# Kernel optimization log

Hardware: AMD Instinct MI355X
Metric: run time of the kernel (lower is better)

Reference implementation:

```python
import jax, jax.numpy as jnp
import numpy as np
from jax.scipy.special import logsumexp
from jax import lax

TARGET_SIZE = 50
TAG_SIZE = TARGET_SIZE + 2  # +2 for START/END tags


def setup_inputs() -> dict:
    key = jax.random.key(0)
    k1, k2 = jax.random.split(key)
    B, L, T = 1024, 512, TAG_SIZE
    feats = jax.random.normal(k1, (B, L, T), dtype=jnp.float32)
    mask = jnp.ones((B, L), dtype=jnp.int32)
    # transitions init per CRF.__init__: zeros, with transitions[:, START]=-1000
    # and transitions[END, :]=-1000 (START=T-2, END=T-1). Add small noise to the
    # trainable part so gradients are non-trivial.
    trans = 0.1 * jax.random.normal(k2, (T, T), dtype=jnp.float32)
    trans = trans.at[:, T - 2].set(-1000.0)  # nothing transitions INTO start
    trans = trans.at[T - 1, :].set(-1000.0)  # nothing transitions OUT of end
    return {"feats": feats, "mask": mask, "transitions": trans}


def reference(feats, mask, transitions):
    # feats: (B, L, T), mask: (B, L) int, transitions: (T, T)
    B, L, T = feats.shape
    START, END = T - 2, T - 1
    # scores[t, b, i, j] = feats[b, t, j] + transitions[i, j]
    # initial partition = scores[0, :, START, :]
    partition0 = feats[:, 0, :] + transitions[START, :]  # (B, T)

    feats_t = jnp.swapaxes(feats[:, 1:, :], 0, 1)   # (L-1, B, T)
    mask_t = jnp.swapaxes(mask[:, 1:], 0, 1)        # (L-1, B)

    def step(part, xs):
        f_t, m_t = xs  # (B, T), (B,)
        # cur[b, i, j] = feats[b,t,j] + transitions[i,j] + partition[b,i]
        cur = f_t[:, None, :] + transitions[None, :, :] + part[:, :, None]
        cur_part = logsumexp(cur, axis=1)  # reduce over previous tag i -> (B, T)
        part = jnp.where((m_t > 0)[:, None], cur_part, part)
        return part, None

    partition, _ = lax.scan(step, partition0, (feats_t, mask_t))

    # final transition step, then select END tag
    final_vals = transitions[None, :, :] + partition[:, :, None]  # (B, T, T)
    final_partition = logsumexp(final_vals, axis=1)[:, END]       # (B,)
    return final_partition.sum()
```

## Files before the change

### kernel.cpp

```cpp
#include <hip/hip_runtime.h>


#define TT 52
#define LL 512
#define NS 8

__device__ __forceinline__ float rl(float x, int lane) {
    return __int_as_float(__builtin_amdgcn_readlane(__float_as_int(x), lane));
}

__global__ void __launch_bounds__(64)
__attribute__((amdgpu_waves_per_eu(1, 1)))
crf_fwd(
    const float* __restrict__ feats,
    const int*   __restrict__ mask,
    const float* __restrict__ trans,
    float*       __restrict__ out)
{
    __shared__ __align__(16) float plds[64];

    const int b = blockIdx.x;
    const int j = threadIdx.x;
    const bool act = (j < TT);
    const int jc = act ? j : 0;

    const float* fb = feats + (size_t)b * LL * TT;
    const int*   mb = mask  + (size_t)b * LL;

    float E[TT];
#pragma unroll
    for (int i = 0; i < TT; ++i) {
        float e = __expf(trans[i * TT + jc]);
        E[i] = act ? e : 0.0f;
    }

    float part0 = act ? (fb[j] + trans[(TT - 2) * TT + j]) : -1.0e30f;
    float shift = rl(part0, 0);
    float pv = act ? __expf(part0 - shift) : 0.0f;

    plds[j] = pv;

    const float4* pq = (const float4*)plds;

    float fpre[NS];
    int   mc[NS];
#pragma unroll
    for (int u = 0; u < NS; ++u) {
        int t = 1 + u;
        fpre[u] = fb[t * TT + jc];
        mc[u]   = mb[t];
    }

    for (int t0 = 1; t0 + NS <= LL; t0 += NS) {
        float fnx[NS];
        int   mn[NS];
#pragma unroll
        for (int u = 0; u < NS; ++u) {
            int tn = t0 + NS + u;
            int tcl = tn < LL ? tn : (LL - 1);
            fnx[u] = fb[tcl * TT + jc];
            mn[u]  = mb[tcl];
        }

        float ef[NS];
#pragma unroll
        for (int u = 0; u < NS; ++u) ef[u] = __expf(fpre[u]);

#pragma unroll
        for (int u = 0; u < NS; ++u) {
            float a0 = 0.f, a1 = 0.f, a2 = 0.f, a3 = 0.f;
#pragma unroll
            for (int k = 0; k < TT / 4; ++k) {
                float4 q = pq[k];
                a0 = fmaf(q.x, E[4 * k + 0], a0);
                a1 = fmaf(q.y, E[4 * k + 1], a1);
                a2 = fmaf(q.z, E[4 * k + 2], a2);
                a3 = fmaf(q.w, E[4 * k + 3], a3);
            }
            float pn = ((a0 + a1) + (a2 + a3)) * ef[u];
            pv = (mc[u] > 0) ? pn : pv;
            if (u == NS - 1) {
                float c = rl(pv, 0);
                shift += __logf(c);
                pv *= __builtin_amdgcn_rcpf(c);
            }
            plds[j] = pv;
        }
#pragma unroll
        for (int u = 0; u < NS; ++u) { fpre[u] = fnx[u]; mc[u] = mn[u]; }
    }

#pragma unroll
    for (int u = 0; u < 7; ++u) {
        float efu = __expf(fpre[u]);
        float a0 = 0.f, a1 = 0.f, a2 = 0.f, a3 = 0.f;
#pragma unroll
        for (int k = 0; k < TT / 4; ++k) {
            float4 q = pq[k];
            a0 = fmaf(q.x, E[4 * k + 0], a0);
            a1 = fmaf(q.y, E[4 * k + 1], a1);
            a2 = fmaf(q.z, E[4 * k + 2], a2);
            a3 = fmaf(q.w, E[4 * k + 3], a3);
        }
        float pn = ((a0 + a1) + (a2 + a3)) * efu;
        pv = (mc[u] > 0) ? pn : pv;
        plds[j] = pv;
    }

    float eend = __expf(trans[jc * TT + (TT - 1)]);
    float val = act ? (eend * pv) : 0.0f;
#pragma unroll
    for (int o = 32; o >= 1; o >>= 1)
        val += __shfl_xor(val, o, 64);
    if (j == 0) atomicAdd(out, __logf(val) + shift);
}

extern "C" void kernel_launch(void* const* d_in, const int* in_sizes, int n_in,
                              void* d_out, int out_size, void* d_ws, size_t ws_size,
                              hipStream_t stream) {
    const float* feats = (const float*)d_in[0];
    const int*   mask  = (const int*)d_in[1];
    const float* trans = (const float*)d_in[2];
    float* out = (float*)d_out;

    const int B = in_sizes[1] / LL;

    hipMemsetAsync(d_out, 0, sizeof(float), stream);
    crf_fwd<<<B, 64, 0, stream>>>(feats, mask, trans, out);
}
```

Baseline: 248.0 us.

## Split CRF recurrence into concurrent forward and backward half-chains meeting at midpoint

Runs the forward partition recurrence and a backward (beta) recurrence at the same time, each covering about half of the sequence, and combines them with a dot product at the midpoint. This halves the serial dependency chain length and gives two independent FMA streams per step to hide LDS and ALU latency. In exchange it doubles the register-held transition matrix (column and row copies), increasing VGPR pressure. It also assumes the backward mask handling matches the reference semantics, which holds for an all-ones mask.

```diff
diff --git a/kernel.cpp b/kernel.cpp
--- a/kernel.cpp
+++ b/kernel.cpp
@@ -17,7 +17,7 @@
     const float* __restrict__ trans,
     float*       __restrict__ out)
 {
-    __shared__ __align__(16) float plds[64];
+    __shared__ __align__(16) float plds[128];
 
     const int b = blockIdx.x;
     const int j = threadIdx.x;
@@ -27,92 +27,150 @@
     const float* fb = feats + (size_t)b * LL * TT;
     const int*   mb = mask  + (size_t)b * LL;
 
-    float E[TT];
+    float Ecol[TT], Erow[TT];
 #pragma unroll
     for (int i = 0; i < TT; ++i) {
-        float e = __expf(trans[i * TT + jc]);
-        E[i] = act ? e : 0.0f;
+        float ec = __expf(trans[i * TT + jc]);
+        float er = __expf(trans[jc * TT + i]);
+        Ecol[i] = act ? ec : 0.0f;
+        Erow[i] = act ? er : 0.0f;
     }
 
     float part0 = act ? (fb[j] + trans[(TT - 2) * TT + j]) : -1.0e30f;
-    float shift = rl(part0, 0);
-    float pv = act ? __expf(part0 - shift) : 0.0f;
+    float shiftF = rl(part0, 0);
+    float pvF = act ? __expf(part0 - shiftF) : 0.0f;
 
-    plds[j] = pv;
+    float wv = act ? __expf(trans[jc * TT + (TT - 1)]) : 0.0f;
+    float shiftB = 0.0f;
 
-    const float4* pq = (const float4*)plds;
+    const float4* pqF = (const float4*)plds;
+    const float4* pqB = (const float4*)(plds + 64);
 
-    float fpre[NS];
-    int   mc[NS];
+    float fpF[NS], fpB[NS];
+    int   mcF[NS], mcB[NS];
 #pragma unroll
     for (int u = 0; u < NS; ++u) {
-        int t = 1 + u;
-        fpre[u] = fb[t * TT + jc];
-        mc[u]   = mb[t];
+        fpF[u] = fb[(1 + u) * TT + jc];
+        mcF[u] = mb[1 + u];
+        fpB[u] = fb[(LL - 1 - u) * TT + jc];
+        mcB[u] = mb[LL - 1 - u];
     }
 
-    for (int t0 = 1; t0 + NS <= LL; t0 += NS) {
-        float fnx[NS];
-        int   mn[NS];
+    for (int g = 0; g + NS <= 248; g += NS) {
+        float fnF[NS], fnB[NS];
+        int   mnF[NS], mnB[NS];
 #pragma unroll
         for (int u = 0; u < NS; ++u) {
-            int tn = t0 + NS + u;
-            int tcl = tn < LL ? tn : (LL - 1);
-            fnx[u] = fb[tcl * TT + jc];
-            mn[u]  = mb[tcl];
+            int kn = g + NS + u;
+            fnF[u] = fb[(1 + kn) * TT + jc];
+            mnF[u] = mb[1 + kn];
+            fnB[u] = fb[(LL - 1 - kn) * TT + jc];
+            mnB[u] = mb[LL - 1 - kn];
         }
 
-        float ef[NS];
+        float efF[NS], efB[NS];
 #pragma unroll
-        for (int u = 0; u < NS; ++u) ef[u] = __expf(fpre[u]);
+        for (int u = 0; u < NS; ++u) {
+            efF[u] = __expf(fpF[u]);
+            efB[u] = __expf(fpB[u]);
+        }
 
 #pragma unroll
         for (int u = 0; u < NS; ++u) {
+            plds[j]      = pvF;
+            plds[64 + j] = efB[u] * wv;
             float a0 = 0.f, a1 = 0.f, a2 = 0.f, a3 = 0.f;
+            float b0 = 0.f, b1 = 0.f, b2 = 0.f, b3 = 0.f;
 #pragma unroll
-            for (int k = 0; k < TT / 4; ++k) {
-                float4 q = pq[k];
-                a0 = fmaf(q.x, E[4 * k + 0], a0);
-                a1 = fmaf(q.y, E[4 * k + 1], a1);
-                a2 = fmaf(q.z, E[4 * k + 2], a2);
-                a3 = fmaf(q.w, E[4 * k + 3], a3);
+            for (int kq = 0; kq < TT / 4; ++kq) {
+                float4 qf = pqF[kq];
+                float4 qb = pqB[kq];
+                a0 = fmaf(qf.x, Ecol[4 * kq + 0], a0);
+                a1 = fmaf(qf.y, Ecol[4 * kq + 1], a1);
+                a2 = fmaf(qf.z, Ecol[4 * kq + 2], a2);
+                a3 = fmaf(qf.w, Ecol[4 * kq + 3], a3);
+                b0 = fmaf(qb.x, Erow[4 * kq + 0], b0);
+                b1 = fmaf(qb.y, Erow[4 * kq + 1], b1);
+                b2 = fmaf(qb.z, Erow[4 * kq + 2], b2);
+                b3 = fmaf(qb.w, Erow[4 * kq + 3], b3);
             }
-            float pn = ((a0 + a1) + (a2 + a3)) * ef[u];
-            pv = (mc[u] > 0) ? pn : pv;
+            float pnF = ((a0 + a1) + (a2 + a3)) * efF[u];
+            float wnB = ((b0 + b1) + (b2 + b3));
+            pvF = (mcF[u] > 0) ? pnF : pvF;
+            wv  = (mcB[u] > 0) ? wnB : wv;
             if (u == NS - 1) {
-                float c = rl(pv, 0);
-                shift += __logf(c);
-                pv *= __builtin_amdgcn_rcpf(c);
+                float cF = rl(pvF, 0);
+                float cB = rl(wv, 0);
+                shiftF += __logf(cF);
+                shiftB += __logf(cB);
+                pvF *= __builtin_amdgcn_rcpf(cF);
+                wv  *= __builtin_amdgcn_rcpf(cB);
             }
-            plds[j] = pv;
         }
 #pragma unroll
-        for (int u = 0; u < NS; ++u) { fpre[u] = fnx[u]; mc[u] = mn[u]; }
+        for (int u = 0; u < NS; ++u) {
+            fpF[u] = fnF[u]; mcF[u] = mnF[u];
+            fpB[u] = fnB[u]; mcB[u] = mnB[u];
+        }
     }
 
 #pragma unroll
     for (int u = 0; u < 7; ++u) {
-        float efu = __expf(fpre[u]);
+        float efFu = __expf(fpF[u]);
+        float efBu = __expf(fpB[u]);
+        plds[j]      = pvF;
+        plds[64 + j] = efBu * wv;
+        float a0 = 0.f, a1 = 0.f, a2 = 0.f, a3 = 0.f;
+        float b0 = 0.f, b1 = 0.f, b2 = 0.f, b3 = 0.f;
+#pragma unroll
+        for (int kq = 0; kq < TT / 4; ++kq) {
+            float4 qf = pqF[kq];
+            float4 qb = pqB[kq];
+            a0 = fmaf(qf.x, Ecol[4 * kq + 0], a0);
+            a1 = fmaf(qf.y, Ecol[4 * kq + 1], a1);
+            a2 = fmaf(qf.z, Ecol[4 * kq + 2], a2);
+            a3 = fmaf(qf.w, Ecol[4 * kq + 3], a3);
+            b0 = fmaf(qb.x, Erow[4 * kq + 0], b0);
+            b1 = fmaf(qb.y, Erow[4 * kq + 1], b1);
+            b2 = fmaf(qb.z, Erow[4 * kq + 2], b2);
+            b3 = fmaf(qb.w, Erow[4 * kq + 3], b3);
+        }
+        float pnF = ((a0 + a1) + (a2 + a3)) * efFu;
+        float wnB = ((b0 + b1) + (b2 + b3));
+        pvF = (mcF[u] > 0) ? pnF : pvF;
+        wv  = (mcB[u] > 0) ? wnB : wv;
+    }
+
+    {
+        float cF = rl(pvF, 0);
+        float cB = rl(wv, 0);
+        shiftF += __logf(cF);
+        shiftB += __logf(cB);
+        pvF *= __builtin_amdgcn_rcpf(cF);
+        wv  *= __builtin_amdgcn_rcpf(cB);
+    }
+
+    {
+        float efFu = __expf(fpF[7]);
+        plds[j] = pvF;
         float a0 = 0.f, a1 = 0.f, a2 = 0.f, a3 = 0.f;
 #pragma unroll
-        for (int k = 0; k < TT / 4; ++k) {
-            float4 q = pq[k];
-            a0 = fmaf(q.x, E[4 * k + 0], a0);
-            a1 = fmaf(q.y, E[4 * k + 1], a1);
-            a2 = fmaf(q.z, E[4 * k + 2], a2);
-            a3 = fmaf(q.w, E[4 * k + 3], a3);
+        for (int kq = 0; kq < TT / 4; ++kq) {
+            float4 qf = pqF[kq];
+            a0 = fmaf(qf.x, Ecol[4 * kq + 0], a0);
+            a1 = fmaf(qf.y, Ecol[4 * kq + 1], a1);
+            a2 = fmaf(qf.z, Ecol[4 * kq + 2], a2);
+            a3 = fmaf(qf.w, Ecol[4 * kq + 3], a3);
         }
-        float pn = ((a0 + a1) + (a2 + a3)) * efu;
-        pv = (mc[u] > 0) ? pn : pv;
-        plds[j] = pv;
+        float pnF = ((a0 + a1) + (a2 + a3)) * efFu;
+        pvF = (mcF[7] > 0) ? pnF : pvF;
     }
 
-    float eend = __expf(trans[jc * TT + (TT - 1)]);
-    float val = act ? (eend * pv) : 0.0f;
+    float val = act ? (pvF * wv) : 0.0f;
 #pragma unroll
     for (int o = 32; o >= 1; o >>= 1)
         val += __shfl_xor(val, o, 64);
-    if (j == 0) atomicAdd(out, __logf(val) + shift);
+    if (j == 0) atomicAdd(out, __logf(val) + shiftF + shiftB);
 }
 
 extern "C" void kernel_launch(void* const* d_in, const int* in_sizes, int n_in,
```

Measured after the change: 243.5 us. Within noise of the previous version (-1.8%).

## Split CRF forward recursion into concurrent forward and backward halves per sequence

Applied to the files above, without the earlier changes.

Each block now runs two wavefronts: one runs the forward recursion over the first half of the sequence, and the other runs a backward (beta) recursion from the END tag over the second half using transposed transitions. The two partial vectors are combined with a dot product after a block barrier. This halves the serial dependency chain per sequence so that two independent chains share a SIMD. In exchange, the block needs twice the threads and registers, and masked-step handling in the backward half relies on the mask being a prefix.

```diff
diff --git a/kernel.cpp b/kernel.cpp
--- a/kernel.cpp
+++ b/kernel.cpp
@@ -4,115 +4,185 @@
 #define TT 52
 #define LL 512
 #define NS 8
+#define KSPLIT 256
 
 __device__ __forceinline__ float rl(float x, int lane) {
     return __int_as_float(__builtin_amdgcn_readlane(__float_as_int(x), lane));
 }
 
-__global__ void __launch_bounds__(64)
-__attribute__((amdgpu_waves_per_eu(1, 1)))
+__global__ void __launch_bounds__(128)
+__attribute__((amdgpu_waves_per_eu(2, 2)))
 crf_fwd(
     const float* __restrict__ feats,
     const int*   __restrict__ mask,
     const float* __restrict__ trans,
     float*       __restrict__ out)
 {
-    __shared__ __align__(16) float plds[64];
-
-    const int b = blockIdx.x;
-    const int j = threadIdx.x;
+    __shared__ __align__(16) float plds[2][64];
+    __shared__ float shsh[2];
+
+    const int b   = blockIdx.x;
+    const int tid = threadIdx.x;
+    const int w   = tid >> 6;
+    const int j   = tid & 63;
     const bool act = (j < TT);
     const int jc = act ? j : 0;
 
     const float* fb = feats + (size_t)b * LL * TT;
     const int*   mb = mask  + (size_t)b * LL;
 
-    float E[TT];
-#pragma unroll
-    for (int i = 0; i < TT; ++i) {
-        float e = __expf(trans[i * TT + jc]);
-        E[i] = act ? e : 0.0f;
+    float pv;
+    float shift;
+
+    if (w == 0) {
+        float E[TT];
+#pragma unroll
+        for (int i = 0; i < TT; ++i) {
+            float e = __expf(trans[i * TT + jc]);
+            E[i] = act ? e : 0.0f;
+        }
+
+        float part0 = act ? (fb[j] + trans[(TT - 2) * TT + j]) : -1.0e30f;
+        shift = rl(part0, 0);
+        pv = act ? __expf(part0 - shift) : 0.0f;
+        plds[0][j] = pv;
+
+        const float4* pq = (const float4*)plds[0];
+
+        float fpre[NS]; int mc[NS];
+#pragma unroll
+        for (int u = 0; u < NS; ++u) {
+            fpre[u] = fb[(1 + u) * TT + jc];
+            mc[u]   = mb[1 + u];
+        }
+
+        for (int t0 = 1; t0 + NS <= KSPLIT + 1; t0 += NS) {
+            float fnx[NS]; int mn[NS];
+#pragma unroll
+            for (int u = 0; u < NS; ++u) {
+                int tn = t0 + NS + u;
+                fnx[u] = fb[tn * TT + jc];
+                mn[u]  = mb[tn];
+            }
+            float ef[NS];
+#pragma unroll
+            for (int u = 0; u < NS; ++u) ef[u] = __expf(fpre[u]);
+
+#pragma unroll
+            for (int u = 0; u < NS; ++u) {
+                float a0 = 0.f, a1 = 0.f, a2 = 0.f, a3 = 0.f;
+#pragma unroll
+                for (int kq = 0; kq < TT / 4; ++kq) {
+                    float4 q = pq[kq];
+                    a0 = fmaf(q.x, E[4 * kq + 0], a0);
+                    a1 = fmaf(q.y, E[4 * kq + 1], a1);
+                    a2 = fmaf(q.z, E[4 * kq + 2], a2);
+                    a3 = fmaf(q.w, E[4 * kq + 3], a3);
+                }
+                float pn = ((a0 + a1) + (a2 + a3)) * ef[u];
+                pv = (mc[u] > 0) ? pn : pv;
+                if (u == NS - 1) {
+                    float c = rl(pv, 0);
+                    shift += __logf(c);
+                    pv *= __builtin_amdgcn_rcpf(c);
+                }
+                plds[0][j] = pv;
+            }
+#pragma unroll
+            for (int u = 0; u < NS; ++u) { fpre[u] = fnx[u]; mc[u] = mn[u]; }
+        }
+    } else {
+        float E[TT];
+#pragma unroll
+        for (int i = 0; i < TT; ++i) {
+            float e = __expf(trans[jc * TT + i]);
+            E[i] = act ? e : 0.0f;
+        }
+
+        pv = act ? __expf(trans[jc * TT + (TT - 1)]) : 0.0f;
+        shift = 0.0f;
+
+        const float4* pq = (const float4*)plds[1];
+
+        float fpre[NS]; int mc[NS];
+#pragma unroll
+        for (int u = 0; u < NS; ++u) {
+            fpre[u] = fb[(LL - 1 - u) * TT + jc];
+            mc[u]   = mb[LL - 1 - u];
+        }
+
+        for (int g = 0; g + NS <= 248; g += NS) {
+            float fnx[NS]; int mn[NS];
+#pragma unroll
+            for (int u = 0; u < NS; ++u) {
+                int kn = g + NS + u;
+                fnx[u] = fb[(LL - 1 - kn) * TT + jc];
+                mn[u]  = mb[LL - 1 - kn];
+            }
+            float ef[NS];
+#pragma unroll
+            for (int u = 0; u < NS; ++u) ef[u] = __expf(fpre[u]);
+
+#pragma unroll
+            for (int u = 0; u < NS; ++u) {
+                plds[1][j] = ef[u] * pv;
+                float a0 = 0.f, a1 = 0.f, a2 = 0.f, a3 = 0.f;
+#pragma unroll
+                for (int kq = 0; kq < TT / 4; ++kq) {
+                    float4 q = pq[kq];
+                    a0 = fmaf(q.x, E[4 * kq + 0], a0);
+                    a1 = fmaf(q.y, E[4 * kq + 1], a1);
+                    a2 = fmaf(q.z, E[4 * kq + 2], a2);
+                    a3 = fmaf(q.w, E[4 * kq + 3], a3);
+                }
+                float pn = ((a0 + a1) + (a2 + a3));
+                pv = (mc[u] > 0) ? pn : pv;
+                if (u == NS - 1) {
+                    float c = rl(pv, 0);
+                    shift += __logf(c);
+                    pv *= __builtin_amdgcn_rcpf(c);
+                }
+            }
+#pragma unroll
+            for (int u = 0; u < NS; ++u) { fpre[u] = fnx[u]; mc[u] = mn[u]; }
+        }
+
+#pragma unroll
+        for (int u = 0; u < 7; ++u) {
+            float efu = __expf(fpre[u]);
+            plds[1][j] = efu * pv;
+            float a0 = 0.f, a1 = 0.f, a2 = 0.f, a3 = 0.f;
+#pragma unroll
+            for (int kq = 0; kq < TT / 4; ++kq) {
+                float4 q = pq[kq];
+                a0 = fmaf(q.x, E[4 * kq + 0], a0);
+                a1 = fmaf(q.y, E[4 * kq + 1], a1);
+                a2 = fmaf(q.z, E[4 * kq + 2], a2);
+                a3 = fmaf(q.w, E[4 * kq + 3], a3);
+            }
+            float pn = ((a0 + a1) + (a2 + a3));
+            pv = (mc[u] > 0) ? pn : pv;
+        }
+
+        {
+            float c = rl(pv, 0);
+            shift += __logf(c);
+            pv *= __builtin_amdgcn_rcpf(c);
+        }
     }
 
-    float part0 = act ? (fb[j] + trans[(TT - 2) * TT + j]) : -1.0e30f;
-    float shift = rl(part0, 0);
-    float pv = act ? __expf(part0 - shift) : 0.0f;
-
-    plds[j] = pv;
-
-    const float4* pq = (const float4*)plds;
-
-    float fpre[NS];
-    int   mc[NS];
-#pragma unroll
-    for (int u = 0; u < NS; ++u) {
-        int t = 1 + u;
-        fpre[u] = fb[t * TT + jc];
-        mc[u]   = mb[t];
+    plds[w][j] = pv;
+    if (j == 0) shsh[w] = shift;
+    __syncthreads();
+
+    if (w == 0) {
+        float wj  = plds[1][j];
+        float val = act ? (pv * wj) : 0.0f;
+#pragma unroll
+        for (int o = 32; o >= 1; o >>= 1)
+            val += __shfl_xor(val, o, 64);
+        if (j == 0) atomicAdd(out, __logf(val) + shift + shsh[1]);
     }
-
-    for (int t0 = 1; t0 + NS <= LL; t0 += NS) {
-        float fnx[NS];
-        int   mn[NS];
-#pragma unroll
-        for (int u = 0; u < NS; ++u) {
-            int tn = t0 + NS + u;
-            int tcl = tn < LL ? tn : (LL - 1);
-            fnx[u] = fb[tcl * TT + jc];
-            mn[u]  = mb[tcl];
-        }
-
-        float ef[NS];
-#pragma unroll
-        for (int u = 0; u < NS; ++u) ef[u] = __expf(fpre[u]);
-
-#pragma unroll
-        for (int u = 0; u < NS; ++u) {
-            float a0 = 0.f, a1 = 0.f, a2 = 0.f, a3 = 0.f;
-#pragma unroll
-            for (int k = 0; k < TT / 4; ++k) {
-                float4 q = pq[k];
-                a0 = fmaf(q.x, E[4 * k + 0], a0);
-                a1 = fmaf(q.y, E[4 * k + 1], a1);
-                a2 = fmaf(q.z, E[4 * k + 2], a2);
-                a3 = fmaf(q.w, E[4 * k + 3], a3);
-            }
-            float pn = ((a0 + a1) + (a2 + a3)) * ef[u];
-            pv = (mc[u] > 0) ? pn : pv;
-            if (u == NS - 1) {
-                float c = rl(pv, 0);
-                shift += __logf(c);
-                pv *= __builtin_amdgcn_rcpf(c);
-            }
-            plds[j] = pv;
-        }
-#pragma unroll
-        for (int u = 0; u < NS; ++u) { fpre[u] = fnx[u]; mc[u] = mn[u]; }
-    }
-
-#pragma unroll
-    for (int u = 0; u < 7; ++u) {
-        float efu = __expf(fpre[u]);
-        float a0 = 0.f, a1 = 0.f, a2 = 0.f, a3 = 0.f;
-#pragma unroll
-        for (int k = 0; k < TT / 4; ++k) {
-            float4 q = pq[k];
-            a0 = fmaf(q.x, E[4 * k + 0], a0);
-            a1 = fmaf(q.y, E[4 * k + 1], a1);
-            a2 = fmaf(q.z, E[4 * k + 2], a2);
-            a3 = fmaf(q.w, E[4 * k + 3], a3);
-        }
-        float pn = ((a0 + a1) + (a2 + a3)) * efu;
-        pv = (mc[u] > 0) ? pn : pv;
-        plds[j] = pv;
-    }
-
-    float eend = __expf(trans[jc * TT + (TT - 1)]);
-    float val = act ? (eend * pv) : 0.0f;
-#pragma unroll
-    for (int o = 32; o >= 1; o >>= 1)
-        val += __shfl_xor(val, o, 64);
-    if (j == 0) atomicAdd(out, __logf(val) + shift);
 }
 
 extern "C" void kernel_launch(void* const* d_in, const int* in_sizes, int n_in,
@@ -126,5 +196,5 @@
     const int B = in_sizes[1] / LL;
 
     hipMemsetAsync(d_out, 0, sizeof(float), stream);
-    crf_fwd<<<B, 64, 0, stream>>>(feats, mask, trans, out);
+    crf_fwd<<<B, 128, 0, stream>>>(feats, mask, trans, out);
 }
```

Measured after the change: 213.7 us. 13.8% less time.
